# Kernel tuning notes

Measured on AMD Instinct MI355X. Metric: run time of the kernel, lower is better.

Reference implementation:

```python
import jax, jax.numpy as jnp
import numpy as np

B, T, HID = 4, 2048, 1024
NH = 16
HS = HID // NH  # 64


def setup_inputs() -> dict:
    key = jax.random.key(0)
    ks = jax.random.split(key, 9)
    s = 1.0 / np.sqrt(HID)
    return {
        "x": jax.random.normal(ks[0], (B, T, HID), dtype=jnp.float32),
        "Wq": jax.random.uniform(ks[1], (HID, HID), jnp.float32, -s, s),
        "bq": jax.random.uniform(ks[2], (HID,), jnp.float32, -s, s),
        "Wk": jax.random.uniform(ks[3], (HID, HID), jnp.float32, -s, s),
        "bk": jax.random.uniform(ks[4], (HID,), jnp.float32, -s, s),
        "Wv": jax.random.uniform(ks[5], (HID, HS), jnp.float32, -s, s),
        "bv": jax.random.uniform(ks[6], (HS,), jnp.float32, -s, s),
        "Wo": jax.random.uniform(ks[7], (HS, HID), jnp.float32, -1.0 / np.sqrt(HS), 1.0 / np.sqrt(HS)),
        "bo": jax.random.uniform(ks[8], (HID,), jnp.float32, -1.0 / np.sqrt(HS), 1.0 / np.sqrt(HS)),
    }


def reference(x, Wq, bq, Wk, bk, Wv, bv, Wo, bo):
    scale = HS ** -0.5
    q = (x @ Wq + bq).reshape(B, T, NH, HS)  # (B,T,H,hs)
    k = (x @ Wk + bk).reshape(B, T, NH, HS)
    v = x @ Wv + bv                          # shared V: (B,T,hs)
    # scores: (B,H,T,T)
    scores = jnp.einsum("bqhd,bkhd->bhqk", q, k) * scale
    attn = jax.nn.softmax(scores, axis=-1)
    attn_avg = attn.mean(axis=1)             # (B,T,T), head-averaged
    out = jnp.einsum("bqk,bkd->bqd", attn_avg, v) @ Wo + bo  # (B,T,HID)
    return out, attn_avg
```

## Files before the change

### kernel.cpp

```cpp
#include <hip/hip_runtime.h>
#include <math.h>

#define Bc   4
#define Tt   2048
#define HIDc 1024
#define NHc  16
#define HSc  64
#define BTc  (Bc * Tt)
#define QSCALE 0.18033688011112042f

typedef __attribute__((ext_vector_type(8))) short bf16x8;
typedef __attribute__((ext_vector_type(4))) float f32x4;

__device__ __forceinline__ unsigned short f2bf(float f) {
    unsigned u = __float_as_uint(f);
    u = u + 0x7FFFu + ((u >> 16) & 1u);
    return (unsigned short)(u >> 16);
}

__device__ __forceinline__ float fexp2(float x) {
#if __has_builtin(__builtin_amdgcn_exp2f)
    return __builtin_amdgcn_exp2f(x);
#else
    float r; asm("v_exp_f32 %0, %1" : "=v"(r) : "v"(x)); return r;
#endif
}

__global__ __launch_bounds__(256) void gemm_f32(
    const float* __restrict__ A, const float* __restrict__ Bm,
    const float* __restrict__ bias, float* __restrict__ C,
    int M, int N, int K)
{
    __shared__ float As[16][64];
    __shared__ float Bs[16][64];

    const int tid  = threadIdx.x;
    const int tx   = tid & 15;
    const int ty   = tid >> 4;
    const int row0 = blockIdx.y * 64;
    const int col0 = blockIdx.x * 64;

    const int la_r = tid >> 2;
    const int la_c = (tid & 3) << 2;
    const int lb_r = tid >> 4;
    const int lb_c = (tid & 15) << 2;

    float acc[4][4] = {};

    for (int k0 = 0; k0 < K; k0 += 16) {
        float4 av = *(const float4*)&A[(long)(row0 + la_r) * K + k0 + la_c];
        float4 bv = *(const float4*)&Bm[(long)(k0 + lb_r) * N + col0 + lb_c];
        __syncthreads();
        As[la_c + 0][la_r] = av.x;
        As[la_c + 1][la_r] = av.y;
        As[la_c + 2][la_r] = av.z;
        As[la_c + 3][la_r] = av.w;
        *(float4*)&Bs[lb_r][lb_c] = bv;
        __syncthreads();
#pragma unroll
        for (int kk = 0; kk < 16; ++kk) {
            float4 a = *(float4*)&As[kk][ty << 2];
            float4 b = *(float4*)&Bs[kk][tx << 2];
            float ar[4] = {a.x, a.y, a.z, a.w};
            float br[4] = {b.x, b.y, b.z, b.w};
#pragma unroll
            for (int i = 0; i < 4; ++i)
#pragma unroll
                for (int j = 0; j < 4; ++j)
                    acc[i][j] = fmaf(ar[i], br[j], acc[i][j]);
        }
    }

    float4 bvv = make_float4(0.f, 0.f, 0.f, 0.f);
    if (bias) bvv = *(const float4*)&bias[col0 + (tx << 2)];
#pragma unroll
    for (int i = 0; i < 4; ++i) {
        int m = row0 + (ty << 2) + i;
        float4 o;
        o.x = acc[i][0] + bvv.x;
        o.y = acc[i][1] + bvv.y;
        o.z = acc[i][2] + bvv.z;
        o.w = acc[i][3] + bvv.w;
        *(float4*)&C[(long)m * N + col0 + (tx << 2)] = o;
    }
}

__global__ __launch_bounds__(256) void init_bias64(
    float* __restrict__ C, const float* __restrict__ bias, long n)
{
    long idx = (long)blockIdx.x * 256 + threadIdx.x;
    if (idx < n) C[idx] = bias ? bias[idx & 63] : 0.f;
}

__global__ __launch_bounds__(256) void cast_bf16(
    const float* __restrict__ src, unsigned short* __restrict__ dst, long n)
{
    long i = ((long)blockIdx.x * 256 + threadIdx.x) * 4;
    if (i >= n) return;
    float4 v = *(const float4*)&src[i];
    ushort4 o;
    o.x = f2bf(v.x); o.y = f2bf(v.y); o.z = f2bf(v.z); o.w = f2bf(v.w);
    *(ushort4*)&dst[i] = o;
}

__global__ __launch_bounds__(256) void transpose_cast(
    const float* __restrict__ W, unsigned short* __restrict__ Wt, int R, int C)
{
    __shared__ float t[32][33];
    const int k0 = blockIdx.x * 32, n0 = blockIdx.y * 32;
    const int c = threadIdx.x & 31, r = threadIdx.x >> 5;
#pragma unroll
    for (int rr = r; rr < 32; rr += 8)
        t[rr][c] = W[(long)(k0 + rr) * C + n0 + c];
    __syncthreads();
#pragma unroll
    for (int rr = r; rr < 32; rr += 8)
        Wt[(long)(n0 + rr) * R + k0 + c] = f2bf(t[c][rr]);
}

__global__ __launch_bounds__(256) void gemm_bt_bf16(
    const unsigned short* __restrict__ A, const unsigned short* __restrict__ Bt,
    const float* __restrict__ bias, unsigned short* __restrict__ C,
    int M, int N, int K, float oscale)
{
    __shared__ unsigned short As[128][72];
    __shared__ unsigned short Bs[128][72];

    const int gid = blockIdx.x;
    const int xcd = gid & 7, ii = gid >> 3;
    const int row0 = (xcd * 8 + (ii >> 3)) * 128;
    const int col0 = (ii & 7) * 128;

    const int tid  = threadIdx.x;
    const int w  = tid >> 6, L = tid & 63;
    const int wm = (w & 1) * 64, wn = (w >> 1) * 64;
    const int lr = tid >> 3;
    const int lc = (tid & 7) * 8;
    const int ml = L & 15, q8 = (L >> 4) * 8, q4 = (L >> 4) * 4;

    f32x4 acc[4][4];
#pragma unroll
    for (int i = 0; i < 4; ++i)
#pragma unroll
        for (int j = 0; j < 4; ++j)
            acc[i][j] = (f32x4){0.f, 0.f, 0.f, 0.f};

    for (int k0 = 0; k0 < K; k0 += 64) {
        __syncthreads();
#pragma unroll
        for (int rr = 0; rr < 128; rr += 32) {
            *(float4*)&As[lr + rr][lc] = *(const float4*)&A[(long)(row0 + lr + rr) * K + k0 + lc];
            *(float4*)&Bs[lr + rr][lc] = *(const float4*)&Bt[(long)(col0 + lr + rr) * K + k0 + lc];
        }
        __syncthreads();
#pragma unroll
        for (int kk = 0; kk < 64; kk += 32) {
            bf16x8 a[4], b[4];
#pragma unroll
            for (int i = 0; i < 4; ++i) a[i] = *(bf16x8*)&As[wm + i * 16 + ml][kk + q8];
#pragma unroll
            for (int j = 0; j < 4; ++j) b[j] = *(bf16x8*)&Bs[wn + j * 16 + ml][kk + q8];
#pragma unroll
            for (int i = 0; i < 4; ++i)
#pragma unroll
                for (int j = 0; j < 4; ++j)
                    acc[i][j] = __builtin_amdgcn_mfma_f32_16x16x32_bf16(a[i], b[j], acc[i][j], 0, 0, 0);
        }
    }

#pragma unroll
    for (int j = 0; j < 4; ++j) {
        const int col = col0 + wn + j * 16 + ml;
        const float bj = bias ? bias[col] : 0.f;
#pragma unroll
        for (int i = 0; i < 4; ++i) {
#pragma unroll
            for (int r = 0; r < 4; ++r) {
                const int row = row0 + wm + i * 16 + q4 + r;
                C[(long)row * N + col] = f2bf((acc[i][j][r] + bj) * oscale);
            }
        }
    }
}

__global__ __launch_bounds__(256) void gemm_v_bf16(
    const unsigned short* __restrict__ A, const unsigned short* __restrict__ Bt,
    float* __restrict__ C)
{
    __shared__ unsigned short As[128][72];
    __shared__ unsigned short Bs[64][72];

    const int gid = blockIdx.x;
    const int xcd = gid & 7, ii = gid >> 3;
    const int row0 = (xcd * 8 + (ii >> 2)) * 128;
    const int kbeg = (ii & 3) * 256;

    const int tid  = threadIdx.x;
    const int w = tid >> 6, L = tid & 63;
    const int ml = L & 15, q8 = (L >> 4) * 8, q4 = (L >> 4) * 4;
    const int ar = tid >> 3, ac = (tid & 7) * 8;
    const int br = tid >> 2, bc = (tid & 3) * 16;

    f32x4 acc[2][4];
#pragma unroll
    for (int i = 0; i < 2; ++i)
#pragma unroll
        for (int j = 0; j < 4; ++j) acc[i][j] = (f32x4){0.f, 0.f, 0.f, 0.f};

    for (int k0 = kbeg; k0 < kbeg + 256; k0 += 64) {
        __syncthreads();
#pragma unroll
        for (int rr = 0; rr < 128; rr += 32)
            *(float4*)&As[ar + rr][ac] = *(const float4*)&A[(long)(row0 + ar + rr) * HIDc + k0 + ac];
        *(float4*)&Bs[br][bc]     = *(const float4*)&Bt[(long)br * HIDc + k0 + bc];
        *(float4*)&Bs[br][bc + 8] = *(const float4*)&Bt[(long)br * HIDc + k0 + bc + 8];
        __syncthreads();
#pragma unroll
        for (int kk = 0; kk < 64; kk += 32) {
            bf16x8 a[2], b[4];
#pragma unroll
            for (int i = 0; i < 2; ++i) a[i] = *(bf16x8*)&As[w * 32 + i * 16 + ml][kk + q8];
#pragma unroll
            for (int j = 0; j < 4; ++j) b[j] = *(bf16x8*)&Bs[j * 16 + ml][kk + q8];
#pragma unroll
            for (int i = 0; i < 2; ++i)
#pragma unroll
                for (int j = 0; j < 4; ++j)
                    acc[i][j] = __builtin_amdgcn_mfma_f32_16x16x32_bf16(a[i], b[j], acc[i][j], 0, 0, 0);
        }
    }

#pragma unroll
    for (int i = 0; i < 2; ++i)
#pragma unroll
        for (int j = 0; j < 4; ++j)
#pragma unroll
            for (int r = 0; r < 4; ++r)
                atomicAdd(&C[(long)(row0 + w * 32 + i * 16 + q4 + r) * 64 + j * 16 + ml], acc[i][j][r]);
}

__global__ __launch_bounds__(256) void attn_denom(
    const unsigned short* __restrict__ qb, const unsigned short* __restrict__ kb,
    float* __restrict__ linv)
{
    const int gid = blockIdx.x;
    const int xcd = gid & 7, ii = gid >> 3;
    const int bh  = xcd * 8 + (ii >> 4);
    const int qt  = ii & 15;
    const int b   = bh >> 4, h = bh & 15;

    __shared__ unsigned short Qs[128][72];
    __shared__ unsigned short Ks[64][72];

    const int tid = threadIdx.x;
    const int w = tid >> 6, L = tid & 63;
    const int ml = L & 15, q8 = (L >> 4) * 8, q4 = (L >> 4) * 4;
    const int ar = tid >> 3, ac = (tid & 7) * 8;
    const int kr = tid >> 2, kc = (tid & 3) * 16;

#pragma unroll
    for (int rr = 0; rr < 128; rr += 32)
        *(float4*)&Qs[ar + rr][ac] =
            *(const float4*)&qb[(long)(b * Tt + qt * 128 + ar + rr) * HIDc + h * HSc + ac];

    const unsigned short* kbase = kb + ((long)(b * Tt + kr) * HIDc + h * HSc + kc);
    float4 v0 = *(const float4*)kbase;
    float4 v1 = *(const float4*)(kbase + 8);

    float lacc[2][4] = {};

    for (int kt = 0; kt < Tt / 64; ++kt) {
        *(float4*)&Ks[kr][kc]     = v0;
        *(float4*)&Ks[kr][kc + 8] = v1;
        if (kt + 1 < Tt / 64) {
            const unsigned short* s = kbase + (long)(kt + 1) * 64 * HIDc;
            v0 = *(const float4*)s;
            v1 = *(const float4*)(s + 8);
        }
        __syncthreads();

        f32x4 acc[2][4];
#pragma unroll
        for (int i = 0; i < 2; ++i)
#pragma unroll
            for (int j = 0; j < 4; ++j) acc[i][j] = (f32x4){0.f, 0.f, 0.f, 0.f};
#pragma unroll
        for (int kk = 0; kk < 64; kk += 32) {
            bf16x8 a[2], bfr[4];
#pragma unroll
            for (int i = 0; i < 2; ++i) a[i] = *(bf16x8*)&Qs[w * 32 + i * 16 + ml][kk + q8];
#pragma unroll
            for (int j = 0; j < 4; ++j) bfr[j] = *(bf16x8*)&Ks[j * 16 + ml][kk + q8];
#pragma unroll
            for (int i = 0; i < 2; ++i)
#pragma unroll
                for (int j = 0; j < 4; ++j)
                    acc[i][j] = __builtin_amdgcn_mfma_f32_16x16x32_bf16(a[i], bfr[j], acc[i][j], 0, 0, 0);
        }
#pragma unroll
        for (int i = 0; i < 2; ++i)
#pragma unroll
            for (int j = 0; j < 4; ++j)
#pragma unroll
                for (int r = 0; r < 4; ++r)
                    lacc[i][r] += fexp2(acc[i][j][r]);
        __syncthreads();
    }

#pragma unroll
    for (int i = 0; i < 2; ++i)
#pragma unroll
        for (int r = 0; r < 4; ++r) {
            float v = lacc[i][r];
            v += __shfl_xor(v, 1, 16);
            v += __shfl_xor(v, 2, 16);
            v += __shfl_xor(v, 4, 16);
            v += __shfl_xor(v, 8, 16);
            if (ml == 0)
                linv[((long)(b * NHc + h)) * Tt + qt * 128 + w * 32 + i * 16 + q4 + r] =
                    1.0f / (v * (float)NHc);
        }
}

__global__ __launch_bounds__(512) void attn_avg_w(
    const unsigned short* __restrict__ qb, const unsigned short* __restrict__ kb,
    const float* __restrict__ linv, const float* __restrict__ v,
    float* __restrict__ attn, float* __restrict__ o1)
{
    const int gid = blockIdx.x;
    const int xcd = gid & 7, ii = gid >> 3;
    const int b = xcd >> 1, qhalf = xcd & 1;
    const int t = ii >> 4, u = ii & 15;
    const int qt  = qhalf * 8 + (t & 1) * 4 + (u >> 2);
    const int ktg = (t >> 1) * 4 + (u & 3);

    __shared__ __align__(16) unsigned char smem[52224];
    unsigned short (*Qs)[72]   = (unsigned short(*)[72])smem;
    unsigned short (*Ks)[72]   = (unsigned short(*)[72])(smem + 18432);
    float (*invsAll)[128]      = (float(*)[128])(smem + 36864);
    unsigned short (*Ps)[136]  = (unsigned short(*)[136])smem;
    unsigned short (*Vst)[136] = (unsigned short(*)[136])(smem + 34816);

    const int tid = threadIdx.x;
    const int w = tid >> 6, L = tid & 63;
    const int ml = L & 15, q8 = (L >> 4) * 8, q4 = (L >> 4) * 4;
    const int wq = (w >> 2) * 64;
    const int wk = (w & 3) * 32;
    const int sr = tid >> 2, sc = (tid & 3) * 16;

    {
        const int hh = tid >> 5, r4 = (tid & 31) * 4;
        *(float4*)&invsAll[hh][r4] =
            *(const float4*)&linv[((long)(b * NHc + hh)) * Tt + qt * 128 + r4];
    }

    const unsigned short* qbase = qb + ((long)(b * Tt + qt * 128 + sr) * HIDc + sc);
    const unsigned short* kbase = kb + ((long)(b * Tt + ktg * 128 + sr) * HIDc + sc);

    float4 qv[2], kv[2];
#pragma unroll
    for (int c = 0; c < 2; ++c) {
        qv[c] = *(const float4*)(qbase + c * 8);
        kv[c] = *(const float4*)(kbase + c * 8);
    }

    float pacc[4][2][4] = {};

    for (int h = 0; h < NHc; ++h) {
#pragma unroll
        for (int c = 0; c < 2; ++c) {
            *(float4*)&Qs[sr][sc + c * 8] = qv[c];
            *(float4*)&Ks[sr][sc + c * 8] = kv[c];
        }
        if (h + 1 < NHc) {
            const unsigned short* sq = qbase + (h + 1) * HSc;
            const unsigned short* sk = kbase + (h + 1) * HSc;
#pragma unroll
            for (int c = 0; c < 2; ++c) {
                qv[c] = *(const float4*)(sq + c * 8);
                kv[c] = *(const float4*)(sk + c * 8);
            }
        }
        __syncthreads();

        f32x4 acc[4][2];
#pragma unroll
        for (int i = 0; i < 4; ++i)
#pragma unroll
            for (int j = 0; j < 2; ++j) acc[i][j] = (f32x4){0.f, 0.f, 0.f, 0.f};
#pragma unroll
        for (int kk = 0; kk < 64; kk += 32) {
            bf16x8 a[4], bfr[2];
#pragma unroll
            for (int i = 0; i < 4; ++i) a[i]   = *(bf16x8*)&Qs[wq + i * 16 + ml][kk + q8];
#pragma unroll
            for (int j = 0; j < 2; ++j) bfr[j] = *(bf16x8*)&Ks[wk + j * 16 + ml][kk + q8];
#pragma unroll
            for (int i = 0; i < 4; ++i)
#pragma unroll
                for (int j = 0; j < 2; ++j)
                    acc[i][j] = __builtin_amdgcn_mfma_f32_16x16x32_bf16(a[i], bfr[j], acc[i][j], 0, 0, 0);
        }
        float ivr[4][4];
#pragma unroll
        for (int i = 0; i < 4; ++i)
            *(float4*)&ivr[i][0] = *(const float4*)&invsAll[h][wq + i * 16 + q4];
#pragma unroll
        for (int i = 0; i < 4; ++i)
#pragma unroll
            for (int j = 0; j < 2; ++j)
#pragma unroll
                for (int r = 0; r < 4; ++r)
                    pacc[i][j][r] += fexp2(acc[i][j][r]) * ivr[i][r];
        __syncthreads();
    }

#pragma unroll
    for (int i = 0; i < 4; ++i)
#pragma unroll
        for (int j = 0; j < 2; ++j)
#pragma unroll
            for (int r = 0; r < 4; ++r) {
                const int qrow = wq + i * 16 + q4 + r;
                const int col  = wk + j * 16 + ml;
                attn[((long)(b * Tt + qt * 128 + qrow)) * Tt + ktg * 128 + col] = pacc[i][j][r];
                Ps[qrow][col] = f2bf(pacc[i][j][r]);
            }
#pragma unroll
    for (int e = tid; e < 8192; e += 512) {
        const int r = e >> 6, d = e & 63;
        Vst[d][r] = f2bf(v[((long)(b * Tt + ktg * 128 + r)) * 64 + d]);
    }
    __syncthreads();

    const int pq = (w >> 1) * 32, wd = (w & 1) * 32;
    f32x4 uacc[2][2];
#pragma unroll
    for (int i = 0; i < 2; ++i)
#pragma unroll
        for (int j = 0; j < 2; ++j) uacc[i][j] = (f32x4){0.f, 0.f, 0.f, 0.f};
#pragma unroll
    for (int kk = 0; kk < 128; kk += 32) {
        bf16x8 a[2], bvv[2];
#pragma unroll
        for (int i = 0; i < 2; ++i) a[i]   = *(bf16x8*)&Ps[pq + i * 16 + ml][kk + q8];
#pragma unroll
        for (int j = 0; j < 2; ++j) bvv[j] = *(bf16x8*)&Vst[wd + j * 16 + ml][kk + q8];
#pragma unroll
        for (int i = 0; i < 2; ++i)
#pragma unroll
            for (int j = 0; j < 2; ++j)
                uacc[i][j] = __builtin_amdgcn_mfma_f32_16x16x32_bf16(a[i], bvv[j], uacc[i][j], 0, 0, 0);
    }
#pragma unroll
    for (int i = 0; i < 2; ++i)
#pragma unroll
        for (int j = 0; j < 2; ++j)
#pragma unroll
            for (int r = 0; r < 4; ++r)
                atomicAdd(&o1[((long)(b * Tt + qt * 128 + pq + i * 16 + q4 + r)) * 64 + wd + j * 16 + ml],
                          uacc[i][j][r]);
}

extern "C" void kernel_launch(void* const* d_in, const int* in_sizes, int n_in,
                              void* d_out, int out_size, void* d_ws, size_t ws_size,
                              hipStream_t stream)
{
    const float* x  = (const float*)d_in[0];
    const float* Wq = (const float*)d_in[1];
    const float* bq = (const float*)d_in[2];
    const float* Wk = (const float*)d_in[3];
    const float* bk = (const float*)d_in[4];
    const float* Wv = (const float*)d_in[5];
    const float* bv = (const float*)d_in[6];
    const float* Wo = (const float*)d_in[7];
    const float* bo = (const float*)d_in[8];

    float* out  = (float*)d_out;
    float* attn = out + (long)BTc * HIDc;

    unsigned short* xb  = (unsigned short*)d_ws;
    unsigned short* Wqt = xb  + (long)BTc * HIDc;
    unsigned short* Wkt = Wqt + (long)HIDc * HIDc;
    unsigned short* Wvt = Wkt + (long)HIDc * HIDc;
    unsigned short* qb  = Wvt + (long)HSc * HIDc;
    unsigned short* kb  = qb  + (long)BTc * HIDc;
    float* v    = (float*)(kb + (long)BTc * HIDc);
    float* linv = v    + (long)BTc * HSc;
    float* o1   = linv + (long)Bc * NHc * Tt;

    dim3 blk(256);

    cast_bf16<<<dim3((BTc * HIDc) / 1024), blk, 0, stream>>>(x, xb, (long)BTc * HIDc);
    transpose_cast<<<dim3(32, 32), blk, 0, stream>>>(Wq, Wqt, HIDc, HIDc);
    transpose_cast<<<dim3(32, 32), blk, 0, stream>>>(Wk, Wkt, HIDc, HIDc);
    transpose_cast<<<dim3(32, 2),  blk, 0, stream>>>(Wv, Wvt, HIDc, HSc);
    init_bias64<<<dim3((BTc * HSc) / 256), blk, 0, stream>>>(v,  bv,      (long)BTc * HSc);
    init_bias64<<<dim3((BTc * HSc) / 256), blk, 0, stream>>>(o1, nullptr, (long)BTc * HSc);

    gemm_bt_bf16<<<dim3(512), blk, 0, stream>>>(xb, Wqt, bq, qb, BTc, HIDc, HIDc, QSCALE);
    gemm_bt_bf16<<<dim3(512), blk, 0, stream>>>(xb, Wkt, bk, kb, BTc, HIDc, HIDc, 1.0f);

    gemm_v_bf16<<<dim3(256), blk, 0, stream>>>(xb, Wvt, v);

    attn_denom<<<dim3(1024), blk, 0, stream>>>(qb, kb, linv);

    attn_avg_w<<<dim3(1024), dim3(512), 0, stream>>>(qb, kb, linv, v, attn, o1);

    gemm_f32<<<dim3(HIDc / 64, BTc / 64), blk, 0, stream>>>(o1, Wo, bo, out, BTc, HIDc, HSc);
}
```

Before: 442.0 us.

## Load MFMA operands directly from global memory, dropping LDS staging and barriers

Both attention kernels stop staging Q/K tiles through shared memory. Each lane now loads its MFMA fragments straight from global memory into registers. The denominator kernel double-buffers K fragments in registers across iterations, and the averaging kernel reads linv directly and drops both per-head __syncthreads. This removes LDS round trips and barrier stalls and lowers LDS use, which could raise occupancy, but it issues redundant global reads across waves that now depend on L2/L1 reuse and uses more registers.

```diff
diff --git a/kernel.cpp b/kernel.cpp
--- a/kernel.cpp
+++ b/kernel.cpp
@@ -249,63 +249,64 @@
     const int qt  = ii & 15;
     const int b   = bh >> 4, h = bh & 15;
 
-    __shared__ unsigned short Qs[128][72];
-    __shared__ unsigned short Ks[64][72];
-
     const int tid = threadIdx.x;
     const int w = tid >> 6, L = tid & 63;
     const int ml = L & 15, q8 = (L >> 4) * 8, q4 = (L >> 4) * 4;
-    const int ar = tid >> 3, ac = (tid & 7) * 8;
-    const int kr = tid >> 2, kc = (tid & 3) * 16;
-
-#pragma unroll
-    for (int rr = 0; rr < 128; rr += 32)
-        *(float4*)&Qs[ar + rr][ac] =
-            *(const float4*)&qb[(long)(b * Tt + qt * 128 + ar + rr) * HIDc + h * HSc + ac];
-
-    const unsigned short* kbase = kb + ((long)(b * Tt + kr) * HIDc + h * HSc + kc);
-    float4 v0 = *(const float4*)kbase;
-    float4 v1 = *(const float4*)(kbase + 8);
+
+    bf16x8 a[2][2];
+#pragma unroll
+    for (int i = 0; i < 2; ++i)
+#pragma unroll
+        for (int s = 0; s < 2; ++s)
+            a[i][s] = *(const bf16x8*)&qb[(long)(b * Tt + qt * 128 + w * 32 + i * 16 + ml) * HIDc
+                                          + h * HSc + s * 32 + q8];
+
+    const unsigned short* kbase = kb + ((long)(b * Tt + ml)) * HIDc + h * HSc + q8;
+
+#define LOADK(dst, kt)                                                          \
+    {                                                                           \
+        _Pragma("unroll")                                                       \
+        for (int j = 0; j < 4; ++j)                                             \
+            _Pragma("unroll")                                                   \
+            for (int s = 0; s < 2; ++s)                                         \
+                dst[j][s] = *(const bf16x8*)(kbase + ((long)((kt) * 64 + j * 16)) * HIDc + s * 32); \
+    }
+
+#define COMPK(src)                                                              \
+    {                                                                           \
+        f32x4 acc[2][4];                                                        \
+        _Pragma("unroll")                                                       \
+        for (int i = 0; i < 2; ++i)                                             \
+            _Pragma("unroll")                                                   \
+            for (int j = 0; j < 4; ++j) acc[i][j] = (f32x4){0.f, 0.f, 0.f, 0.f};\
+        _Pragma("unroll")                                                       \
+        for (int s = 0; s < 2; ++s)                                             \
+            _Pragma("unroll")                                                   \
+            for (int i = 0; i < 2; ++i)                                         \
+                _Pragma("unroll")                                               \
+                for (int j = 0; j < 4; ++j)                                     \
+                    acc[i][j] = __builtin_amdgcn_mfma_f32_16x16x32_bf16(        \
+                        a[i][s], src[j][s], acc[i][j], 0, 0, 0);                \
+        _Pragma("unroll")                                                       \
+        for (int i = 0; i < 2; ++i)                                             \
+            _Pragma("unroll")                                                   \
+            for (int j = 0; j < 4; ++j)                                         \
+                _Pragma("unroll")                                               \
+                for (int r = 0; r < 4; ++r)                                     \
+                    lacc[i][r] += fexp2(acc[i][j][r]);                          \
+    }
 
     float lacc[2][4] = {};
-
-    for (int kt = 0; kt < Tt / 64; ++kt) {
-        *(float4*)&Ks[kr][kc]     = v0;
-        *(float4*)&Ks[kr][kc + 8] = v1;
-        if (kt + 1 < Tt / 64) {
-            const unsigned short* s = kbase + (long)(kt + 1) * 64 * HIDc;
-            v0 = *(const float4*)s;
-            v1 = *(const float4*)(s + 8);
-        }
-        __syncthreads();
-
-        f32x4 acc[2][4];
-#pragma unroll
-        for (int i = 0; i < 2; ++i)
-#pragma unroll
-            for (int j = 0; j < 4; ++j) acc[i][j] = (f32x4){0.f, 0.f, 0.f, 0.f};
-#pragma unroll
-        for (int kk = 0; kk < 64; kk += 32) {
-            bf16x8 a[2], bfr[4];
-#pragma unroll
-            for (int i = 0; i < 2; ++i) a[i] = *(bf16x8*)&Qs[w * 32 + i * 16 + ml][kk + q8];
-#pragma unroll
-            for (int j = 0; j < 4; ++j) bfr[j] = *(bf16x8*)&Ks[j * 16 + ml][kk + q8];
-#pragma unroll
-            for (int i = 0; i < 2; ++i)
-#pragma unroll
-                for (int j = 0; j < 4; ++j)
-                    acc[i][j] = __builtin_amdgcn_mfma_f32_16x16x32_bf16(a[i], bfr[j], acc[i][j], 0, 0, 0);
-        }
-#pragma unroll
-        for (int i = 0; i < 2; ++i)
-#pragma unroll
-            for (int j = 0; j < 4; ++j)
-#pragma unroll
-                for (int r = 0; r < 4; ++r)
-                    lacc[i][r] += fexp2(acc[i][j][r]);
-        __syncthreads();
-    }
+    bf16x8 bA[4][2], bB[4][2];
+    LOADK(bA, 0);
+    for (int kt = 0; kt < 32; kt += 2) {
+        LOADK(bB, kt + 1);
+        COMPK(bA);
+        if (kt + 2 < 32) LOADK(bA, kt + 2);
+        COMPK(bB);
+    }
+#undef LOADK
+#undef COMPK
 
 #pragma unroll
     for (int i = 0; i < 2; ++i)
@@ -334,54 +335,32 @@
     const int qt  = qhalf * 8 + (t & 1) * 4 + (u >> 2);
     const int ktg = (t >> 1) * 4 + (u & 3);
 
-    __shared__ __align__(16) unsigned char smem[52224];
-    unsigned short (*Qs)[72]   = (unsigned short(*)[72])smem;
-    unsigned short (*Ks)[72]   = (unsigned short(*)[72])(smem + 18432);
-    float (*invsAll)[128]      = (float(*)[128])(smem + 36864);
-    unsigned short (*Ps)[136]  = (unsigned short(*)[136])smem;
-    unsigned short (*Vst)[136] = (unsigned short(*)[136])(smem + 34816);
+    __shared__ unsigned short Ps[128][136];
+    __shared__ unsigned short Vst[64][136];
 
     const int tid = threadIdx.x;
     const int w = tid >> 6, L = tid & 63;
     const int ml = L & 15, q8 = (L >> 4) * 8, q4 = (L >> 4) * 4;
     const int wq = (w >> 2) * 64;
     const int wk = (w & 3) * 32;
-    const int sr = tid >> 2, sc = (tid & 3) * 16;
-
-    {
-        const int hh = tid >> 5, r4 = (tid & 31) * 4;
-        *(float4*)&invsAll[hh][r4] =
-            *(const float4*)&linv[((long)(b * NHc + hh)) * Tt + qt * 128 + r4];
-    }
-
-    const unsigned short* qbase = qb + ((long)(b * Tt + qt * 128 + sr) * HIDc + sc);
-    const unsigned short* kbase = kb + ((long)(b * Tt + ktg * 128 + sr) * HIDc + sc);
-
-    float4 qv[2], kv[2];
-#pragma unroll
-    for (int c = 0; c < 2; ++c) {
-        qv[c] = *(const float4*)(qbase + c * 8);
-        kv[c] = *(const float4*)(kbase + c * 8);
-    }
+
+    const long qr0 = (long)(b * Tt + qt * 128 + wq);
+    const long kr0 = (long)(b * Tt + ktg * 128 + wk);
 
     float pacc[4][2][4] = {};
 
     for (int h = 0; h < NHc; ++h) {
-#pragma unroll
-        for (int c = 0; c < 2; ++c) {
-            *(float4*)&Qs[sr][sc + c * 8] = qv[c];
-            *(float4*)&Ks[sr][sc + c * 8] = kv[c];
-        }
-        if (h + 1 < NHc) {
-            const unsigned short* sq = qbase + (h + 1) * HSc;
-            const unsigned short* sk = kbase + (h + 1) * HSc;
-#pragma unroll
-            for (int c = 0; c < 2; ++c) {
-                qv[c] = *(const float4*)(sq + c * 8);
-                kv[c] = *(const float4*)(sk + c * 8);
-            }
-        }
-        __syncthreads();
+        bf16x8 a[4][2], bf[2][2];
+#pragma unroll
+        for (int i = 0; i < 4; ++i)
+#pragma unroll
+            for (int s = 0; s < 2; ++s)
+                a[i][s] = *(const bf16x8*)&qb[(qr0 + i * 16 + ml) * HIDc + h * HSc + s * 32 + q8];
+#pragma unroll
+        for (int j = 0; j < 2; ++j)
+#pragma unroll
+            for (int s = 0; s < 2; ++s)
+                bf[j][s] = *(const bf16x8*)&kb[(kr0 + j * 16 + ml) * HIDc + h * HSc + s * 32 + q8];
 
         f32x4 acc[4][2];
 #pragma unroll
@@ -389,22 +368,18 @@
 #pragma unroll
             for (int j = 0; j < 2; ++j) acc[i][j] = (f32x4){0.f, 0.f, 0.f, 0.f};
 #pragma unroll
-        for (int kk = 0; kk < 64; kk += 32) {
-            bf16x8 a[4], bfr[2];
-#pragma unroll
-            for (int i = 0; i < 4; ++i) a[i]   = *(bf16x8*)&Qs[wq + i * 16 + ml][kk + q8];
-#pragma unroll
-            for (int j = 0; j < 2; ++j) bfr[j] = *(bf16x8*)&Ks[wk + j * 16 + ml][kk + q8];
+        for (int s = 0; s < 2; ++s)
 #pragma unroll
             for (int i = 0; i < 4; ++i)
 #pragma unroll
                 for (int j = 0; j < 2; ++j)
-                    acc[i][j] = __builtin_amdgcn_mfma_f32_16x16x32_bf16(a[i], bfr[j], acc[i][j], 0, 0, 0);
-        }
+                    acc[i][j] = __builtin_amdgcn_mfma_f32_16x16x32_bf16(a[i][s], bf[j][s], acc[i][j], 0, 0, 0);
+
         float ivr[4][4];
 #pragma unroll
         for (int i = 0; i < 4; ++i)
-            *(float4*)&ivr[i][0] = *(const float4*)&invsAll[h][wq + i * 16 + q4];
+            *(float4*)&ivr[i][0] =
+                *(const float4*)&linv[((long)(b * NHc + h)) * Tt + qt * 128 + wq + i * 16 + q4];
 #pragma unroll
         for (int i = 0; i < 4; ++i)
 #pragma unroll
@@ -412,7 +387,6 @@
 #pragma unroll
                 for (int r = 0; r < 4; ++r)
                     pacc[i][j][r] += fexp2(acc[i][j][r]) * ivr[i][r];
-        __syncthreads();
     }
 
 #pragma unroll
@@ -441,16 +415,16 @@
         for (int j = 0; j < 2; ++j) uacc[i][j] = (f32x4){0.f, 0.f, 0.f, 0.f};
 #pragma unroll
     for (int kk = 0; kk < 128; kk += 32) {
-        bf16x8 a[2], bvv[2];
-#pragma unroll
-        for (int i = 0; i < 2; ++i) a[i]   = *(bf16x8*)&Ps[pq + i * 16 + ml][kk + q8];
+        bf16x8 a2[2], bvv[2];
+#pragma unroll
+        for (int i = 0; i < 2; ++i) a2[i]  = *(bf16x8*)&Ps[pq + i * 16 + ml][kk + q8];
 #pragma unroll
         for (int j = 0; j < 2; ++j) bvv[j] = *(bf16x8*)&Vst[wd + j * 16 + ml][kk + q8];
 #pragma unroll
         for (int i = 0; i < 2; ++i)
 #pragma unroll
             for (int j = 0; j < 2; ++j)
-                uacc[i][j] = __builtin_amdgcn_mfma_f32_16x16x32_bf16(a[i], bvv[j], uacc[i][j], 0, 0, 0);
+                uacc[i][j] = __builtin_amdgcn_mfma_f32_16x16x32_bf16(a2[i], bvv[j], uacc[i][j], 0, 0, 0);
     }
 #pragma unroll
     for (int i = 0; i < 2; ++i)
```

Result: slower. 536.8 us (+21.4%).
